# Kernel optimization log

Measured on AMD Instinct MI355X. Metric: run time of the kernel, lower is better.

The kernel has to match this reference:

```python
import jax, jax.numpy as jnp
import numpy as np

TEMP = 1.0

def setup_inputs() -> dict:
    key = jax.random.key(0)
    k1, k2, k3 = jax.random.split(key, 3)
    B, C, H, W = 8, 256, 64, 64
    h = jax.random.normal(k1, (B, C, H, W), dtype=jnp.float32)
    xs = jax.random.normal(k2, (B, C, H, W), dtype=jnp.float32)
    ys = jax.random.normal(k3, (B, C, H, W), dtype=jnp.float32)
    return {"h": h, "xs": xs, "ys": ys}

def reference(h, xs, ys):
    B, C, H, W = h.shape
    Bs, Cs, Hs, Ws = xs.shape
    hf = h.reshape(B, C, H * W)            # [B, C, N]   N = H*W
    xf = xs.reshape(Bs, Cs, Hs * Ws)       # [B, C, M]   M = Hs*Ws
    yf = ys.reshape(ys.shape[0], ys.shape[1], -1)  # [B, C, M]
    # attention[b, n, m] = sum_c h[b,c,n] * xs[b,c,m]
    attn = jnp.einsum('bcn,bcm->bnm', hf, xf)
    attn = jax.nn.softmax(attn / TEMP, axis=2)  # softmax over support positions m
    # xxs[b, c, n] = sum_m ys[b,c,m] * attn[b,n,m]
    xxs = jnp.einsum('bcm,bnm->bcn', yf, attn)
    return xxs.reshape(B, C, H, W)
```

## Files before the change

kernel.cpp:

```cpp
#include <hip/hip_runtime.h>
#include <stdint.h>

#define B_ 8
#define C_ 256
#define N_ 4096
#define M_ 4096
#define NT 64
#define MT 64
#define PP 72

typedef _Float16 f16x8 __attribute__((ext_vector_type(8)));
typedef _Float16 f16x4 __attribute__((ext_vector_type(4)));
typedef float f32x4 __attribute__((ext_vector_type(4)));

__device__ __forceinline__ void async16(const _Float16* g, _Float16* l) {
    __builtin_amdgcn_global_load_lds(
        (const __attribute__((address_space(1))) void*)g,
        (__attribute__((address_space(3))) void*)l, 16, 0, 0);
}

__global__ __launch_bounds__(256) void kTranspose(const float* __restrict__ xs,
                                                  _Float16* __restrict__ kt) {
    __shared__ float tile[64][65];
    int b = blockIdx.z, m0 = blockIdx.x * 64, c0 = blockIdx.y * 64;
    int t = threadIdx.x;
    int cl = t >> 4, m4 = (t & 15) * 4;
#pragma unroll
    for (int i = 0; i < 4; i++) {
        int c = c0 + cl + i * 16;
        const float4 v = *(const float4*)(xs + ((size_t)(b * C_ + c) * M_) + m0 + m4);
        tile[m4 + 0][cl + i * 16] = v.x;
        tile[m4 + 1][cl + i * 16] = v.y;
        tile[m4 + 2][cl + i * 16] = v.z;
        tile[m4 + 3][cl + i * 16] = v.w;
    }
    __syncthreads();
    int ml = t >> 4, c4 = (t & 15) * 4;
#pragma unroll
    for (int i = 0; i < 4; i++) {
        int m = m0 + ml + i * 16;
        f16x4 o;
        o[0] = (_Float16)tile[ml + i * 16][c4 + 0];
        o[1] = (_Float16)tile[ml + i * 16][c4 + 1];
        o[2] = (_Float16)tile[ml + i * 16][c4 + 2];
        o[3] = (_Float16)tile[ml + i * 16][c4 + 3];
        *(f16x4*)(kt + ((size_t)(b * M_ + m) * C_) + c0 + c4) = o;
    }
}

__global__ __launch_bounds__(256) void kConvert(const float* __restrict__ ys,
                                                _Float16* __restrict__ vb) {
    size_t i = ((size_t)blockIdx.x * 256 + threadIdx.x) * 4;
    float4 v = *(const float4*)(ys + i);
    f16x4 o;
    o[0] = (_Float16)v.x; o[1] = (_Float16)v.y;
    o[2] = (_Float16)v.z; o[3] = (_Float16)v.w;
    *(f16x4*)(vb + i) = o;
}

__global__ __launch_bounds__(256, 2) void kAttn(const float* __restrict__ h,
                                                const _Float16* __restrict__ kt,
                                                const _Float16* __restrict__ vb,
                                                float* __restrict__ out) {
    __shared__ _Float16 sK[MT * 256];
    __shared__ _Float16 sV[C_ * 64];
    __shared__ _Float16 sP[NT * PP];
    __shared__ float sAlpha[NT];
    __shared__ float sL[NT];

    const int t = threadIdx.x;
    const int w = t >> 6, lane = t & 63, quad = lane >> 4, l15 = lane & 15;
    const int bx = blockIdx.x;
    const int b = bx >> 6;
    const int n0 = (bx & 63) * NT;

    const int nb = w * 16;
    const int cb = w * 64;

    {
        int cl = t >> 4, n4 = (t & 15) * 4;
        for (int i = 0; i < 16; i++) {
            int c = i * 16 + cl;
            const float4 v = *(const float4*)(h + ((size_t)(b * C_ + c) * N_) + n0 + n4);
            float xv[4] = {v.x, v.y, v.z, v.w};
#pragma unroll
            for (int j = 0; j < 4; j++) {
                int row = n4 + j;
                sK[row * 256 + (((c >> 3) ^ (row & 31)) << 3) + (c & 7)] = (_Float16)xv[j];
            }
        }
    }
    __syncthreads();

    f16x8 qf[8];
    {
        int qrow = nb + l15;
#pragma unroll
        for (int ks = 0; ks < 8; ks++)
            qf[ks] = *(const f16x8*)(sK + qrow * 256 + ((((ks << 2) + quad) ^ (qrow & 31)) << 3));
    }

    f32x4 o[4][4];
#pragma unroll
    for (int i = 0; i < 4; i++)
#pragma unroll
        for (int j = 0; j < 4; j++)
            o[i][j] = (f32x4){0.f, 0.f, 0.f, 0.f};

    float mst[4], lst[4];
#pragma unroll
    for (int r = 0; r < 4; r++) { mst[r] = -3.0e38f; lst[r] = 0.f; }

    const _Float16* srcKb = kt + (size_t)b * M_ * C_;
    const _Float16* srcVb = vb + (size_t)b * C_ * M_;

    for (int m0i = 0; m0i < M_; m0i += MT) {
        __syncthreads();

        {
            const _Float16* srcK = srcKb + (size_t)m0i * C_;
#pragma unroll
            for (int j = 0; j < 8; j++) {
                int row = w * 16 + j * 2 + (lane >> 5);
                int logi = (lane & 31) ^ (row & 31);
                async16(srcK + (size_t)row * C_ + logi * 8, sK + (w * 16 + j * 2) * 256);
            }
#pragma unroll
            for (int j = 0; j < 8; j++) {
                int row = w * 64 + j * 8 + (lane >> 3);
                int logi = (lane & 7) ^ (row & 7);
                async16(srcVb + (size_t)row * M_ + m0i + logi * 8, sV + (w * 64 + j * 8) * 64);
            }
        }
        __syncthreads();

        f32x4 s[4];
#pragma unroll
        for (int mt = 0; mt < 4; mt++) s[mt] = (f32x4){0.f, 0.f, 0.f, 0.f};
#pragma unroll
        for (int ks = 0; ks < 8; ks++) {
#pragma unroll
            for (int mt = 0; mt < 4; mt++) {
                int krow = mt * 16 + l15;
                f16x8 bk = *(const f16x8*)(sK + krow * 256 + ((((ks << 2) + quad) ^ (krow & 31)) << 3));
                s[mt] = __builtin_amdgcn_mfma_f32_16x16x32_f16(qf[ks], bk, s[mt], 0, 0, 0);
            }
        }

#pragma unroll
        for (int r = 0; r < 4; r++) {
            float rowmax = fmaxf(fmaxf(s[0][r], s[1][r]), fmaxf(s[2][r], s[3][r]));
#pragma unroll
            for (int off = 1; off < 16; off <<= 1)
                rowmax = fmaxf(rowmax, __shfl_xor(rowmax, off, 64));
            float mnew = fmaxf(mst[r], rowmax);
            float al = exp2f((mst[r] - mnew) * 1.44269504f);
            float rowsum = 0.f;
#pragma unroll
            for (int mt = 0; mt < 4; mt++) {
                float p = exp2f((s[mt][r] - mnew) * 1.44269504f);
                s[mt][r] = p;
                rowsum += p;
            }
#pragma unroll
            for (int off = 1; off < 16; off <<= 1)
                rowsum += __shfl_xor(rowsum, off, 64);
            lst[r] = lst[r] * al + rowsum;
            mst[r] = mnew;
            int row = nb + quad * 4 + r;
            if (l15 == 0) sAlpha[row] = al;
#pragma unroll
            for (int mt = 0; mt < 4; mt++)
                sP[row * PP + mt * 16 + l15] = (_Float16)s[mt][r];
        }
        __syncthreads();

        float av[4];
#pragma unroll
        for (int nt = 0; nt < 4; nt++) av[nt] = sAlpha[nt * 16 + l15];
#pragma unroll
        for (int ct = 0; ct < 4; ct++)
#pragma unroll
            for (int nt = 0; nt < 4; nt++) {
                o[ct][nt][0] *= av[nt];
                o[ct][nt][1] *= av[nt];
                o[ct][nt][2] *= av[nt];
                o[ct][nt][3] *= av[nt];
            }
#pragma unroll
        for (int ks = 0; ks < 2; ks++) {
            f16x8 aV[4];
#pragma unroll
            for (int ct = 0; ct < 4; ct++) {
                int vrow = cb + ct * 16 + l15;
                aV[ct] = *(const f16x8*)(sV + vrow * 64 + ((((ks << 2) + quad) ^ (vrow & 7)) << 3));
            }
#pragma unroll
            for (int nt = 0; nt < 4; nt++) {
                f16x8 bp = *(const f16x8*)(sP + (nt * 16 + l15) * PP + ks * 32 + quad * 8);
#pragma unroll
                for (int ct = 0; ct < 4; ct++)
                    o[ct][nt] = __builtin_amdgcn_mfma_f32_16x16x32_f16(aV[ct], bp, o[ct][nt], 0, 0, 0);
            }
        }
    }

    if (l15 == 0) {
#pragma unroll
        for (int r = 0; r < 4; r++) sL[nb + quad * 4 + r] = lst[r];
    }
    __syncthreads();
    float linv[4];
#pragma unroll
    for (int nt = 0; nt < 4; nt++) linv[nt] = 1.0f / sL[nt * 16 + l15];
#pragma unroll
    for (int ct = 0; ct < 4; ct++)
#pragma unroll
        for (int nt = 0; nt < 4; nt++)
#pragma unroll
            for (int r = 0; r < 4; r++) {
                int c = cb + ct * 16 + quad * 4 + r;
                out[((size_t)(b * C_ + c)) * N_ + n0 + nt * 16 + l15] = o[ct][nt][r] * linv[nt];
            }
}

extern "C" void kernel_launch(void* const* d_in, const int* in_sizes, int n_in,
                              void* d_out, int out_size, void* d_ws, size_t ws_size,
                              hipStream_t stream) {
    const float* h  = (const float*)d_in[0];
    const float* xs = (const float*)d_in[1];
    const float* ys = (const float*)d_in[2];
    float* out = (float*)d_out;

    _Float16* kt  = (_Float16*)d_ws;
    _Float16* vbb = kt + (size_t)B_ * M_ * C_;

    kTranspose<<<dim3(M_ / 64, C_ / 64, B_), 256, 0, stream>>>(xs, kt);
    kConvert<<<dim3((B_ * C_ * M_) / (4 * 256)), 256, 0, stream>>>(ys, vbb);
    kAttn<<<dim3(B_ * (N_ / NT)), 256, 0, stream>>>(h, kt, vbb, out);
}
```

Before: 380.3 us.

## Double-buffer K tiles, load V directly to registers, skip unneeded rescales, merge prep kernels

Merges the transpose and convert kernels into one launch. In the attention kernel, K tiles are double-buffered in LDS so the next tile's async load overlaps the current compute. V fragments are now read straight from global memory into registers instead of going through LDS. The row-sum shuffle reduction moves out of the loop to the end, and the output rescale is skipped when no row max changed, tracked with a shared flag and atomicOr. The trade-offs are uncoalesced per-lane global V loads and possibly higher register pressure, plus an extra atomic and a branch.

```diff
diff --git a/kernel.cpp b/kernel.cpp
--- a/kernel.cpp
+++ b/kernel.cpp
@@ -8,6 +8,7 @@
 #define NT 64
 #define MT 64
 #define PP 72
+#define L2E 1.44269504f
 
 typedef _Float16 f16x8 __attribute__((ext_vector_type(8)));
 typedef _Float16 f16x4 __attribute__((ext_vector_type(4)));
@@ -19,63 +20,69 @@
         (__attribute__((address_space(3))) void*)l, 16, 0, 0);
 }
 
-__global__ __launch_bounds__(256) void kTranspose(const float* __restrict__ xs,
-                                                  _Float16* __restrict__ kt) {
-    __shared__ float tile[64][65];
-    int b = blockIdx.z, m0 = blockIdx.x * 64, c0 = blockIdx.y * 64;
+__global__ __launch_bounds__(256) void kPre(const float* __restrict__ xs,
+                                            const float* __restrict__ ys,
+                                            _Float16* __restrict__ kt,
+                                            _Float16* __restrict__ vb) {
+    int bx = blockIdx.x;
     int t = threadIdx.x;
-    int cl = t >> 4, m4 = (t & 15) * 4;
-#pragma unroll
-    for (int i = 0; i < 4; i++) {
-        int c = c0 + cl + i * 16;
-        const float4 v = *(const float4*)(xs + ((size_t)(b * C_ + c) * M_) + m0 + m4);
-        tile[m4 + 0][cl + i * 16] = v.x;
-        tile[m4 + 1][cl + i * 16] = v.y;
-        tile[m4 + 2][cl + i * 16] = v.z;
-        tile[m4 + 3][cl + i * 16] = v.w;
-    }
-    __syncthreads();
-    int ml = t >> 4, c4 = (t & 15) * 4;
-#pragma unroll
-    for (int i = 0; i < 4; i++) {
-        int m = m0 + ml + i * 16;
+    if (bx < 2048) {
+        __shared__ float tile[64][65];
+        int b = bx >> 8, rem = bx & 255;
+        int c0 = (rem >> 6) * 64, m0 = (rem & 63) * 64;
+        int cl = t >> 4, m4 = (t & 15) * 4;
+#pragma unroll
+        for (int i = 0; i < 4; i++) {
+            int c = c0 + cl + i * 16;
+            const float4 v = *(const float4*)(xs + ((size_t)(b * C_ + c) * M_) + m0 + m4);
+            tile[m4 + 0][cl + i * 16] = v.x;
+            tile[m4 + 1][cl + i * 16] = v.y;
+            tile[m4 + 2][cl + i * 16] = v.z;
+            tile[m4 + 3][cl + i * 16] = v.w;
+        }
+        __syncthreads();
+        int ml = t >> 4, c4 = (t & 15) * 4;
+#pragma unroll
+        for (int i = 0; i < 4; i++) {
+            int m = m0 + ml + i * 16;
+            f16x4 o;
+            o[0] = (_Float16)tile[ml + i * 16][c4 + 0];
+            o[1] = (_Float16)tile[ml + i * 16][c4 + 1];
+            o[2] = (_Float16)tile[ml + i * 16][c4 + 2];
+            o[3] = (_Float16)tile[ml + i * 16][c4 + 3];
+            *(f16x4*)(kt + ((size_t)(b * M_ + m) * C_) + c0 + c4) = o;
+        }
+    } else {
+        size_t i = ((size_t)(bx - 2048) * 256 + t) * 4;
+        float4 v = *(const float4*)(ys + i);
         f16x4 o;
-        o[0] = (_Float16)tile[ml + i * 16][c4 + 0];
-        o[1] = (_Float16)tile[ml + i * 16][c4 + 1];
-        o[2] = (_Float16)tile[ml + i * 16][c4 + 2];
-        o[3] = (_Float16)tile[ml + i * 16][c4 + 3];
-        *(f16x4*)(kt + ((size_t)(b * M_ + m) * C_) + c0 + c4) = o;
-    }
-}
-
-__global__ __launch_bounds__(256) void kConvert(const float* __restrict__ ys,
-                                                _Float16* __restrict__ vb) {
-    size_t i = ((size_t)blockIdx.x * 256 + threadIdx.x) * 4;
-    float4 v = *(const float4*)(ys + i);
-    f16x4 o;
-    o[0] = (_Float16)v.x; o[1] = (_Float16)v.y;
-    o[2] = (_Float16)v.z; o[3] = (_Float16)v.w;
-    *(f16x4*)(vb + i) = o;
+        o[0] = (_Float16)v.x; o[1] = (_Float16)v.y;
+        o[2] = (_Float16)v.z; o[3] = (_Float16)v.w;
+        *(f16x4*)(vb + i) = o;
+    }
 }
 
 __global__ __launch_bounds__(256, 2) void kAttn(const float* __restrict__ h,
                                                 const _Float16* __restrict__ kt,
                                                 const _Float16* __restrict__ vb,
                                                 float* __restrict__ out) {
-    __shared__ _Float16 sK[MT * 256];
-    __shared__ _Float16 sV[C_ * 64];
+    __shared__ _Float16 sK[2][MT * 256];
     __shared__ _Float16 sP[NT * PP];
     __shared__ float sAlpha[NT];
     __shared__ float sL[NT];
+    __shared__ int sFlag[2];
 
     const int t = threadIdx.x;
     const int w = t >> 6, lane = t & 63, quad = lane >> 4, l15 = lane & 15;
-    const int bx = blockIdx.x;
-    const int b = bx >> 6;
-    const int n0 = (bx & 63) * NT;
-
+    const int b = blockIdx.x >> 6;
+    const int n0 = (blockIdx.x & 63) * NT;
     const int nb = w * 16;
     const int cb = w * 64;
+
+    const _Float16* srcKb = kt + (size_t)b * M_ * C_;
+    const _Float16* srcVb = vb + (size_t)b * C_ * M_;
+
+    if (t == 0) { sFlag[0] = 0; sFlag[1] = 0; }
 
     {
         int cl = t >> 4, n4 = (t & 15) * 4;
@@ -86,8 +93,14 @@
 #pragma unroll
             for (int j = 0; j < 4; j++) {
                 int row = n4 + j;
-                sK[row * 256 + (((c >> 3) ^ (row & 31)) << 3) + (c & 7)] = (_Float16)xv[j];
-            }
+                sK[1][row * 256 + (((c >> 3) ^ (row & 31)) << 3) + (c & 7)] = (_Float16)xv[j];
+            }
+        }
+#pragma unroll
+        for (int j = 0; j < 8; j++) {
+            int row = w * 16 + j * 2 + (lane >> 5);
+            int logi = (lane & 31) ^ (row & 31);
+            async16(srcKb + (size_t)row * C_ + logi * 8, &sK[0][(w * 16 + j * 2) * 256]);
         }
     }
     __syncthreads();
@@ -97,7 +110,7 @@
         int qrow = nb + l15;
 #pragma unroll
         for (int ks = 0; ks < 8; ks++)
-            qf[ks] = *(const f16x8*)(sK + qrow * 256 + ((((ks << 2) + quad) ^ (qrow & 31)) << 3));
+            qf[ks] = *(const f16x8*)(&sK[1][qrow * 256 + ((((ks << 2) + quad) ^ (qrow & 31)) << 3)]);
     }
 
     f32x4 o[4][4];
@@ -107,32 +120,35 @@
         for (int j = 0; j < 4; j++)
             o[i][j] = (f32x4){0.f, 0.f, 0.f, 0.f};
 
-    float mst[4], lst[4];
-#pragma unroll
-    for (int r = 0; r < 4; r++) { mst[r] = -3.0e38f; lst[r] = 0.f; }
-
-    const _Float16* srcKb = kt + (size_t)b * M_ * C_;
-    const _Float16* srcVb = vb + (size_t)b * C_ * M_;
-
-    for (int m0i = 0; m0i < M_; m0i += MT) {
+    float mst[4], lp[4];
+#pragma unroll
+    for (int r = 0; r < 4; r++) { mst[r] = -3.0e38f; lp[r] = 0.f; }
+
+    for (int it = 0; it < M_ / MT; it++) {
+        const int cur = it & 1, nxt = cur ^ 1;
+        const int m0i = it * MT;
         __syncthreads();
 
-        {
-            const _Float16* srcK = srcKb + (size_t)m0i * C_;
+        if (t == 0) sFlag[nxt] = 0;
+
+        if (it + 1 < M_ / MT) {
+            const _Float16* srcK = srcKb + (size_t)(m0i + MT) * C_;
 #pragma unroll
             for (int j = 0; j < 8; j++) {
                 int row = w * 16 + j * 2 + (lane >> 5);
                 int logi = (lane & 31) ^ (row & 31);
-                async16(srcK + (size_t)row * C_ + logi * 8, sK + (w * 16 + j * 2) * 256);
-            }
-#pragma unroll
-            for (int j = 0; j < 8; j++) {
-                int row = w * 64 + j * 8 + (lane >> 3);
-                int logi = (lane & 7) ^ (row & 7);
-                async16(srcVb + (size_t)row * M_ + m0i + logi * 8, sV + (w * 64 + j * 8) * 64);
-            }
-        }
-        __syncthreads();
+                async16(srcK + (size_t)row * C_ + logi * 8, &sK[nxt][(w * 16 + j * 2) * 256]);
+            }
+        }
+
+        f16x8 vf[2][4];
+#pragma unroll
+        for (int ks = 0; ks < 2; ks++)
+#pragma unroll
+            for (int ct = 0; ct < 4; ct++) {
+                int vrow = cb + ct * 16 + l15;
+                vf[ks][ct] = *(const f16x8*)(srcVb + (size_t)vrow * M_ + m0i + ks * 32 + quad * 8);
+            }
 
         f32x4 s[4];
 #pragma unroll
@@ -142,7 +158,7 @@
 #pragma unroll
             for (int mt = 0; mt < 4; mt++) {
                 int krow = mt * 16 + l15;
-                f16x8 bk = *(const f16x8*)(sK + krow * 256 + ((((ks << 2) + quad) ^ (krow & 31)) << 3));
+                f16x8 bk = *(const f16x8*)(&sK[cur][krow * 256 + ((((ks << 2) + quad) ^ (krow & 31)) << 3)]);
                 s[mt] = __builtin_amdgcn_mfma_f32_16x16x32_f16(qf[ks], bk, s[mt], 0, 0, 0);
             }
         }
@@ -153,61 +169,63 @@
 #pragma unroll
             for (int off = 1; off < 16; off <<= 1)
                 rowmax = fmaxf(rowmax, __shfl_xor(rowmax, off, 64));
-            float mnew = fmaxf(mst[r], rowmax);
-            float al = exp2f((mst[r] - mnew) * 1.44269504f);
-            float rowsum = 0.f;
+            float al = 1.0f;
+            if (rowmax > mst[r]) {
+                al = exp2f((mst[r] - rowmax) * L2E);
+                mst[r] = rowmax;
+            }
+            float psum = 0.f;
 #pragma unroll
             for (int mt = 0; mt < 4; mt++) {
-                float p = exp2f((s[mt][r] - mnew) * 1.44269504f);
+                float p = exp2f((s[mt][r] - mst[r]) * L2E);
                 s[mt][r] = p;
-                rowsum += p;
-            }
-#pragma unroll
-            for (int off = 1; off < 16; off <<= 1)
-                rowsum += __shfl_xor(rowsum, off, 64);
-            lst[r] = lst[r] * al + rowsum;
-            mst[r] = mnew;
+                psum += p;
+            }
+            lp[r] = lp[r] * al + psum;
             int row = nb + quad * 4 + r;
-            if (l15 == 0) sAlpha[row] = al;
+            if (l15 == 0) {
+                sAlpha[row] = al;
+                if (al != 1.0f) atomicOr(&sFlag[cur], 1);
+            }
 #pragma unroll
             for (int mt = 0; mt < 4; mt++)
                 sP[row * PP + mt * 16 + l15] = (_Float16)s[mt][r];
         }
         __syncthreads();
 
-        float av[4];
-#pragma unroll
-        for (int nt = 0; nt < 4; nt++) av[nt] = sAlpha[nt * 16 + l15];
-#pragma unroll
-        for (int ct = 0; ct < 4; ct++)
-#pragma unroll
-            for (int nt = 0; nt < 4; nt++) {
-                o[ct][nt][0] *= av[nt];
-                o[ct][nt][1] *= av[nt];
-                o[ct][nt][2] *= av[nt];
-                o[ct][nt][3] *= av[nt];
-            }
+        if (sFlag[cur]) {
+            float av[4];
+#pragma unroll
+            for (int nt = 0; nt < 4; nt++) av[nt] = sAlpha[nt * 16 + l15];
+#pragma unroll
+            for (int ct = 0; ct < 4; ct++)
+#pragma unroll
+                for (int nt = 0; nt < 4; nt++) {
+                    o[ct][nt][0] *= av[nt];
+                    o[ct][nt][1] *= av[nt];
+                    o[ct][nt][2] *= av[nt];
+                    o[ct][nt][3] *= av[nt];
+                }
+        }
+
 #pragma unroll
         for (int ks = 0; ks < 2; ks++) {
-            f16x8 aV[4];
-#pragma unroll
-            for (int ct = 0; ct < 4; ct++) {
-                int vrow = cb + ct * 16 + l15;
-                aV[ct] = *(const f16x8*)(sV + vrow * 64 + ((((ks << 2) + quad) ^ (vrow & 7)) << 3));
-            }
 #pragma unroll
             for (int nt = 0; nt < 4; nt++) {
                 f16x8 bp = *(const f16x8*)(sP + (nt * 16 + l15) * PP + ks * 32 + quad * 8);
 #pragma unroll
                 for (int ct = 0; ct < 4; ct++)
-                    o[ct][nt] = __builtin_amdgcn_mfma_f32_16x16x32_f16(aV[ct], bp, o[ct][nt], 0, 0, 0);
-            }
-        }
-    }
-
-    if (l15 == 0) {
-#pragma unroll
-        for (int r = 0; r < 4; r++) sL[nb + quad * 4 + r] = lst[r];
+                    o[ct][nt] = __builtin_amdgcn_mfma_f32_16x16x32_f16(vf[ks][ct], bp, o[ct][nt], 0, 0, 0);
+            }
+        }
+    }
+
+#pragma unroll
+    for (int r = 0; r < 4; r++) {
+#pragma unroll
+        for (int off = 1; off < 16; off <<= 1)
+            lp[r] += __shfl_xor(lp[r], off, 64);
+        if (l15 == 0) sL[nb + quad * 4 + r] = lp[r];
     }
     __syncthreads();
     float linv[4];
@@ -235,7 +253,6 @@
     _Float16* kt  = (_Float16*)d_ws;
     _Float16* vbb = kt + (size_t)B_ * M_ * C_;
 
-    kTranspose<<<dim3(M_ / 64, C_ / 64, B_), 256, 0, stream>>>(xs, kt);
-    kConvert<<<dim3((B_ * C_ * M_) / (4 * 256)), 256, 0, stream>>>(ys, vbb);
+    kPre<<<dim3(2048 + 8192), 256, 0, stream>>>(xs, ys, kt, vbb);
     kAttn<<<dim3(B_ * (N_ / NT)), 256, 0, stream>>>(h, kt, vbb, out);
 }
```

Result: faster. 356.7 us (-6.2%).
